# Kernel optimization log

Measured on AMD Instinct MI355X. Metric: run time of the kernel, lower is better.

## Reference

```python
import jax, jax.numpy as jnp
import numpy as np

USER_NUM = 100000
ITEM_NUM = 50000
E = 128   # embedding_size
A = 64    # attention_size
M = 8     # memory_size
B = 4096  # batch
NF = 50   # friends per user


def _l2norm(x, axis):
    # torch F.normalize(p=2): x / max(||x||, eps)
    n = jnp.sqrt(jnp.sum(x * x, axis=axis, keepdims=True))
    return x / jnp.maximum(n, 1e-12)


def setup_inputs() -> dict:
    key = jax.random.key(0)
    ks = jax.random.split(key, 9)
    u = lambda k, shape: jax.random.uniform(k, shape, jnp.float32, -0.1, 0.1)
    return {
        "input_u": jax.random.randint(ks[0], (B,), 0, USER_NUM),
        "input_i": jax.random.randint(ks[1], (B,), 0, ITEM_NUM),
        "input_uf": jax.random.randint(ks[2], (B, NF), 0, USER_NUM + 1),
        "uidW": u(ks[3], (USER_NUM + 1, E)),
        "iidW": u(ks[4], (ITEM_NUM, E)),
        "i_bias": jnp.zeros((ITEM_NUM,), jnp.float32),
        "Key": u(ks[5], (E, M)),
        "Mem": jnp.ones((M, E), jnp.float32),
        "WA": u(ks[6], (E, A)),
        "BA": jnp.zeros((A,), jnp.float32),
        "U_omega": u(ks[7], (A, 1)),
    }


def reference(input_u, input_i, input_uf, uidW, iidW, i_bias, Key, Mem, WA, BA, U_omega):
    user_num = uidW.shape[0] - 1  # padding id
    uid = uidW[input_u]                      # [B, E]
    iid = iidW[input_i]                      # [B, E]
    i_b = i_bias[input_i]                    # [B]
    fe = uidW[input_uf]                      # [B, F, E] friend embeddings
    fn = (input_uf != user_num).astype(uid.dtype)  # [B, F] valid-friend mask

    fe = fn[:, :, None] * fe
    uid_n = _l2norm(uid, axis=1)
    fe_n = _l2norm(fe, axis=2)
    cross = uid_n[:, None, :] * fe_n                     # [B, F, E]
    att_key = jnp.einsum('bfe,em->bfm', cross, Key)      # [B, F, M]
    att_mem = jax.nn.softmax(att_key, axis=0)            # softmax over batch (faithful to dim=0)
    att_mem = fn[:, :, None] * att_mem
    f1 = jnp.einsum('bfm,me->bfe', att_mem, Mem)         # [B, F, E]
    f2 = f1 * fe
    h = jax.nn.relu(jnp.einsum('bfe,ea->bfa', f2, WA) + BA)
    j = jnp.exp(jnp.einsum('bfa,ao->bfo', h, U_omega))   # [B, F, 1]
    j = fn[:, :, None] * j
    w = j / (jnp.sum(j, axis=1, keepdims=True) + 1e-8)
    friend = jnp.sum(w * f2, axis=1)                     # [B, E] (dropout p=0 -> identity)
    user = uid + friend
    score = jnp.sum(user * iid, axis=1) + i_b            # [B]
    return score
```

## Files before the change

### kernel.cpp

```cpp
#include <hip/hip_runtime.h>

#define EDIM 128
#define MDIM 8
#define ADIM 64
#define NFR  50
#define NCOL (NFR * MDIM)
#define NPART 64

typedef __attribute__((ext_vector_type(8))) short short8;
typedef __attribute__((ext_vector_type(4))) float f32x4;

__device__ __forceinline__ float waveReduceSum(float v) {
    #pragma unroll
    for (int s = 32; s >= 1; s >>= 1) v += __shfl_xor(v, s, 64);
    return v;
}
__device__ __forceinline__ short f2bf(float x) {
    unsigned u = __float_as_uint(x);
    u += 0x7FFFu + ((u >> 16) & 1u);
    return (short)(u >> 16);
}
__device__ __forceinline__ float bf2f(short s) {
    return __uint_as_float(((unsigned)(unsigned short)s) << 16);
}

__global__ __launch_bounds__(256)
void k0_prep(const float* __restrict__ WA, const float* __restrict__ Mem,
             const float* __restrict__ Key,
             short* __restrict__ WATf, short* __restrict__ MemTf,
             short* __restrict__ KeyTf, float* __restrict__ S)
{
    int t = blockIdx.x * 256 + threadIdx.x;
    int lane = t & 63, c = lane & 15, g = (lane >> 4) & 3;
    short8 v = {0, 0, 0, 0, 0, 0, 0, 0};
    if (t < 1024) {
        int frag = t >> 6, Ma = frag >> 2, Kt = frag & 3;
        int a = Ma * 16 + c;
        #pragma unroll
        for (int j = 0; j < 8; ++j) {
            int e = Kt * 32 + g * 8 + j;
            v[j] = f2bf(WA[(size_t)e * ADIM + a]);
        }
        *(short8*)(WATf + (size_t)t * 8) = v;
    } else if (t < 1536) {
        int i = t - 1024, Mt = i >> 6;
        int e = Mt * 16 + c;
        #pragma unroll
        for (int j = 0; j < 8; ++j) {
            int k = g * 8 + j;
            v[j] = (k < MDIM) ? f2bf(Mem[(size_t)k * EDIM + e]) : (short)0;
        }
        *(short8*)(MemTf + (size_t)i * 8) = v;
    } else if (t < 1792) {
        int i = t - 1536, Kt = i >> 6;
        #pragma unroll
        for (int j = 0; j < 8; ++j) {
            int e = Kt * 32 + g * 8 + j;
            v[j] = (c < MDIM) ? f2bf(Key[(size_t)e * MDIM + c]) : (short)0;
        }
        *(short8*)(KeyTf + (size_t)i * 8) = v;
    } else if (t < 1792 + NCOL) {
        S[t - 1792] = 0.f;
    }
}

__global__ __launch_bounds__(256, 6)
void k1_attkey(const int* __restrict__ input_u, const int* __restrict__ input_uf,
               const float* __restrict__ uidW, const short* __restrict__ KeyTf,
               float* __restrict__ eatt, short* __restrict__ feB, int user_num)
{
    const int b = blockIdx.x, t = threadIdx.x, w = t >> 6, l = t & 63;
    const int c = l & 15, g = l >> 4;
    __shared__ float uidn[EDIM];
    __shared__ float redW[4];
    __shared__ int ufL[64];

    if (t < 64) ufL[t] = (t < NFR) ? input_uf[(size_t)b * NFR + t] : user_num;
    const int u = input_u[b];
    float x = (t < EDIM) ? uidW[(size_t)u * EDIM + t] : 0.f;
    float ss = waveReduceSum(x * x);
    if (l == 0) redW[w] = ss;
    __syncthreads();
    float uinv = 1.0f / fmaxf(sqrtf(redW[0] + redW[1] + redW[2] + redW[3]), 1e-12f);
    if (t < EDIM) uidn[t] = x * uinv;
    __syncthreads();

    const int f = w * 16 + c;
    const int fid = ufL[f];
    const float fn = (f < NFR && fid != user_num) ? 1.0f : 0.0f;
    const float* fp = uidW + (size_t)fid * EDIM;

    float4 fe[4][2];
    #pragma unroll
    for (int Kt = 0; Kt < 4; ++Kt) {
        fe[Kt][0] = *(const float4*)(fp + Kt * 32 + g * 8);
        fe[Kt][1] = *(const float4*)(fp + Kt * 32 + g * 8 + 4);
    }
    float fss = 0.f;
    #pragma unroll
    for (int Kt = 0; Kt < 4; ++Kt)
        #pragma unroll
        for (int h = 0; h < 2; ++h) {
            float4 q = fe[Kt][h];
            fss += q.x * q.x + q.y * q.y + q.z * q.z + q.w * q.w;
        }
    fss += __shfl_xor(fss, 16, 64);
    fss += __shfl_xor(fss, 32, 64);
    const float inv2 = fn / fmaxf(sqrtf(fss), 1e-12f);

    short* fbb = feB + (size_t)b * 8192;
    f32x4 acc = {0.f, 0.f, 0.f, 0.f};
    #pragma unroll
    for (int Kt = 0; Kt < 4; ++Kt) {
        short8 fo;
        fo[0] = f2bf(fe[Kt][0].x * fn); fo[1] = f2bf(fe[Kt][0].y * fn);
        fo[2] = f2bf(fe[Kt][0].z * fn); fo[3] = f2bf(fe[Kt][0].w * fn);
        fo[4] = f2bf(fe[Kt][1].x * fn); fo[5] = f2bf(fe[Kt][1].y * fn);
        fo[6] = f2bf(fe[Kt][1].z * fn); fo[7] = f2bf(fe[Kt][1].w * fn);
        *(short8*)(fbb + f * 128 + Kt * 32 + g * 8) = fo;

        float4 un0 = *(const float4*)&uidn[Kt * 32 + g * 8];
        float4 un1 = *(const float4*)&uidn[Kt * 32 + g * 8 + 4];
        short8 bf;
        bf[0] = f2bf(un0.x * fe[Kt][0].x * inv2);
        bf[1] = f2bf(un0.y * fe[Kt][0].y * inv2);
        bf[2] = f2bf(un0.z * fe[Kt][0].z * inv2);
        bf[3] = f2bf(un0.w * fe[Kt][0].w * inv2);
        bf[4] = f2bf(un1.x * fe[Kt][1].x * inv2);
        bf[5] = f2bf(un1.y * fe[Kt][1].y * inv2);
        bf[6] = f2bf(un1.z * fe[Kt][1].z * inv2);
        bf[7] = f2bf(un1.w * fe[Kt][1].w * inv2);
        short8 af = *(const short8*)(KeyTf + (size_t)(Kt * 64 + l) * 8);
        acc = __builtin_amdgcn_mfma_f32_16x16x32_bf16(af, bf, acc, 0, 0, 0);
    }
    if (f < NFR && g < 2) {
        float4 st = {__expf(acc[0]), __expf(acc[1]), __expf(acc[2]), __expf(acc[3])};
        *(float4*)&eatt[(size_t)b * NCOL + f * MDIM + g * 4] = st;
    }
}

__global__ __launch_bounds__(256)
void k2a_sum(const float* __restrict__ eatt, float* __restrict__ S, int B)
{
    const int blk = blockIdx.x, t = threadIdx.x, w = t >> 6, l = t & 63;
    __shared__ float colS[4][NCOL];
    const int rowsPerBlk = B / NPART;
    const int rowsPerWave = rowsPerBlk >> 2;
    const int r0 = blk * rowsPerBlk + w * rowsPerWave;

    float4 a1 = {0.f, 0.f, 0.f, 0.f}, a2 = {0.f, 0.f, 0.f, 0.f};
    for (int it = 0; it < rowsPerWave; ++it) {
        const float* row = eatt + (size_t)(r0 + it) * NCOL;
        float4 v1 = *(const float4*)(row + 4 * l);
        a1.x += v1.x; a1.y += v1.y; a1.z += v1.z; a1.w += v1.w;
        if (l < 36) {
            float4 v2 = *(const float4*)(row + 256 + 4 * l);
            a2.x += v2.x; a2.y += v2.y; a2.z += v2.z; a2.w += v2.w;
        }
    }
    *(float4*)&colS[w][4 * l] = a1;
    if (l < 36) *(float4*)&colS[w][256 + 4 * l] = a2;
    __syncthreads();
    for (int i = t; i < NCOL; i += 256)
        atomicAdd(&S[i], colS[0][i] + colS[1][i] + colS[2][i] + colS[3][i]);
}

__global__ __launch_bounds__(256, 6)
void k3_final(const int* __restrict__ input_u, const int* __restrict__ input_i,
              const int* __restrict__ input_uf, const float* __restrict__ uidW,
              const float* __restrict__ iidW, const float* __restrict__ i_bias,
              const short* __restrict__ WATf, const short* __restrict__ MemTf,
              const float* __restrict__ BA, const float* __restrict__ U_omega,
              const float* __restrict__ eatt, const float* __restrict__ S,
              const short* __restrict__ feB, float* __restrict__ out,
              int user_num)
{
    const int b = blockIdx.x, t = threadIdx.x, w = t >> 6, l = t & 63;
    const int c = l & 15, g = l >> 4;
    __shared__ short f2s[4][4 * 64 * 8];
    __shared__ float uidL[EDIM], iidL[EDIM];
    __shared__ float baL[ADIM], uoL[ADIM];
    __shared__ int ufL[64];
    __shared__ float sjW[4], syW[4];

    if (t < 64) ufL[t] = (t < NFR) ? input_uf[(size_t)b * NFR + t] : user_num;
    const int u = input_u[b];
    const int ii = input_i[b];
    if (t < EDIM) {
        uidL[t] = uidW[(size_t)u * EDIM + t];
        iidL[t] = iidW[(size_t)ii * EDIM + t];
    }
    if (t < ADIM) { baL[t] = BA[t]; uoL[t] = U_omega[t]; }
    __syncthreads();

    const int f = w * 16 + c;
    const float fn = (f < NFR && ufL[f] != user_num) ? 1.0f : 0.0f;
    const short* fbb = feB + (size_t)b * 8192;

    short8 amf = {0, 0, 0, 0, 0, 0, 0, 0};
    if (g == 0 && fn > 0.f) {
        const float* ea = eatt + (size_t)b * NCOL + f * 8;
        float4 e0 = *(const float4*)ea;
        float4 e1 = *(const float4*)(ea + 4);
        float4 s0 = *(const float4*)&S[f * 8];
        float4 s1 = *(const float4*)&S[f * 8 + 4];
        amf[0] = f2bf(e0.x * __builtin_amdgcn_rcpf(s0.x));
        amf[1] = f2bf(e0.y * __builtin_amdgcn_rcpf(s0.y));
        amf[2] = f2bf(e0.z * __builtin_amdgcn_rcpf(s0.z));
        amf[3] = f2bf(e0.w * __builtin_amdgcn_rcpf(s0.w));
        amf[4] = f2bf(e1.x * __builtin_amdgcn_rcpf(s1.x));
        amf[5] = f2bf(e1.y * __builtin_amdgcn_rcpf(s1.y));
        amf[6] = f2bf(e1.z * __builtin_amdgcn_rcpf(s1.z));
        amf[7] = f2bf(e1.w * __builtin_amdgcn_rcpf(s1.w));
    }

    f32x4 C1[8];
    #pragma unroll
    for (int Mt = 0; Mt < 8; ++Mt) {
        short8 af = *(const short8*)(MemTf + (size_t)(Mt * 64 + l) * 8);
        f32x4 z = {0.f, 0.f, 0.f, 0.f};
        C1[Mt] = __builtin_amdgcn_mfma_f32_16x16x32_bf16(af, amf, z, 0, 0, 0);
    }

    #pragma unroll
    for (int Mt = 0; Mt < 8; ++Mt) {
        uint2 fv = *(const uint2*)(fbb + f * 128 + Mt * 16 + g * 4);
        float q0 = C1[Mt][0] * bf2f((short)(fv.x & 0xFFFF));
        float q1 = C1[Mt][1] * bf2f((short)(fv.x >> 16));
        float q2 = C1[Mt][2] * bf2f((short)(fv.y & 0xFFFF));
        float q3 = C1[Mt][3] * bf2f((short)(fv.y >> 16));
        unsigned d0 = ((unsigned)(unsigned short)f2bf(q0)) |
                      (((unsigned)(unsigned short)f2bf(q1)) << 16);
        unsigned d1 = ((unsigned)(unsigned short)f2bf(q2)) |
                      (((unsigned)(unsigned short)f2bf(q3)) << 16);
        int lane2 = ((Mt & 1) * 2 + (g >> 1)) * 16 + c;
        int off = ((Mt >> 1) * 64 + lane2) * 8 + (g & 1) * 4;
        uint2 dd = {d0, d1};
        *(uint2*)&f2s[w][off] = dd;
    }

    f32x4 C2[4], C3 = {0.f, 0.f, 0.f, 0.f};
    #pragma unroll
    for (int Ma = 0; Ma < 4; ++Ma) C2[Ma] = (f32x4){0.f, 0.f, 0.f, 0.f};
    #pragma unroll
    for (int Kt = 0; Kt < 4; ++Kt) {
        short8 bf = *(const short8*)&f2s[w][(Kt * 64 + l) * 8];
        #pragma unroll
        for (int Ma = 0; Ma < 4; ++Ma) {
            short8 af = *(const short8*)(WATf + (size_t)((Ma * 4 + Kt) * 64 + l) * 8);
            C2[Ma] = __builtin_amdgcn_mfma_f32_16x16x32_bf16(af, bf, C2[Ma], 0, 0, 0);
        }
        short8 itf = {0, 0, 0, 0, 0, 0, 0, 0};
        if (c == 0) {
            float4 i0 = *(const float4*)&iidL[Kt * 32 + g * 8];
            float4 i1 = *(const float4*)&iidL[Kt * 32 + g * 8 + 4];
            itf[0] = f2bf(i0.x); itf[1] = f2bf(i0.y);
            itf[2] = f2bf(i0.z); itf[3] = f2bf(i0.w);
            itf[4] = f2bf(i1.x); itf[5] = f2bf(i1.y);
            itf[6] = f2bf(i1.z); itf[7] = f2bf(i1.w);
        }
        C3 = __builtin_amdgcn_mfma_f32_16x16x32_bf16(itf, bf, C3, 0, 0, 0);
    }

    float psum = 0.f;
    #pragma unroll
    for (int Ma = 0; Ma < 4; ++Ma) {
        float4 ba4 = *(const float4*)&baL[Ma * 16 + g * 4];
        float4 uo4 = *(const float4*)&uoL[Ma * 16 + g * 4];
        psum += fmaxf(C2[Ma][0] + ba4.x, 0.f) * uo4.x;
        psum += fmaxf(C2[Ma][1] + ba4.y, 0.f) * uo4.y;
        psum += fmaxf(C2[Ma][2] + ba4.z, 0.f) * uo4.z;
        psum += fmaxf(C2[Ma][3] + ba4.w, 0.f) * uo4.w;
    }
    psum += __shfl_xor(psum, 16, 64);
    psum += __shfl_xor(psum, 32, 64);
    const float jv = (fn > 0.f) ? __expf(psum) : 0.f;
    const float jy = jv * C3[0];
    float sj = waveReduceSum((g == 0) ? jv : 0.f);
    float sy = waveReduceSum(jy);
    if (l == 0) { sjW[w] = sj; syW[w] = sy; }
    __syncthreads();

    if (w == 0) {
        float s = uidL[l] * iidL[l] + uidL[l + 64] * iidL[l + 64];
        s = waveReduceSum(s);
        if (l == 0) {
            float Sj = sjW[0] + sjW[1] + sjW[2] + sjW[3] + 1e-8f;
            float Sy = syW[0] + syW[1] + syW[2] + syW[3];
            out[b] = s + Sy / Sj + i_bias[ii];
        }
    }
}

extern "C" void kernel_launch(void* const* d_in, const int* in_sizes, int n_in,
                              void* d_out, int out_size, void* d_ws, size_t ws_size,
                              hipStream_t stream)
{
    const int*   input_u  = (const int*)d_in[0];
    const int*   input_i  = (const int*)d_in[1];
    const int*   input_uf = (const int*)d_in[2];
    const float* uidW     = (const float*)d_in[3];
    const float* iidW     = (const float*)d_in[4];
    const float* i_bias   = (const float*)d_in[5];
    const float* Key      = (const float*)d_in[6];
    const float* Mem      = (const float*)d_in[7];
    const float* WA       = (const float*)d_in[8];
    const float* BA       = (const float*)d_in[9];
    const float* U_om     = (const float*)d_in[10];

    const int B = in_sizes[0];
    const int user_num = in_sizes[3] / EDIM - 1;

    float* eatt = (float*)d_ws;
    float* S    = eatt + (size_t)B * NCOL;
    short* WATf  = (short*)(S + NCOL);
    short* MemTf = WATf + 16 * 64 * 8;
    short* KeyTf = MemTf + 8 * 64 * 8;
    short* feB   = KeyTf + 4 * 64 * 8;

    k0_prep<<<9, 256, 0, stream>>>(WA, Mem, Key, WATf, MemTf, KeyTf, S);
    k1_attkey<<<B, 256, 0, stream>>>(input_u, input_uf, uidW, KeyTf, eatt, feB, user_num);
    k2a_sum<<<NPART, 256, 0, stream>>>(eatt, S, B);
    k3_final<<<B, 256, 0, stream>>>(input_u, input_i, input_uf, uidW, iidW, i_bias,
                                    WATf, MemTf, BA, U_om, eatt, S, feB,
                                    (float*)d_out, user_num);
}
```

Before: 187.9 us.

## Pre-convert user embedding table to bf16 and gather from it instead of staging feB

A new prep stage converts the whole user embedding table to bf16 on every call. Both the attention-key kernel and the final kernel then gather friend embeddings directly from that bf16 table. This removes the large per-batch feB buffer that one kernel wrote and the other read back, and it halves the bytes of every gather. In exchange, each call streams the full table once for conversion, and the user's own embedding is now read in bf16, which slightly lowers precision. The occupancy hint for k1 also goes from 6 to 8.

```diff
diff --git a/kernel.cpp b/kernel.cpp
--- a/kernel.cpp
+++ b/kernel.cpp
@@ -25,12 +25,26 @@
 }
 
 __global__ __launch_bounds__(256)
-void k0_prep(const float* __restrict__ WA, const float* __restrict__ Mem,
-             const float* __restrict__ Key,
-             short* __restrict__ WATf, short* __restrict__ MemTf,
-             short* __restrict__ KeyTf, float* __restrict__ S)
-{
-    int t = blockIdx.x * 256 + threadIdx.x;
+void k0_all(const float* __restrict__ uidW, const float* __restrict__ WA,
+            const float* __restrict__ Mem, const float* __restrict__ Key,
+            short* __restrict__ ubW, short* __restrict__ WATf,
+            short* __restrict__ MemTf, short* __restrict__ KeyTf,
+            float* __restrict__ S, int nU, int cvtBlocks)
+{
+    int blk = blockIdx.x;
+    if (blk < cvtBlocks) {
+        int idx = (blk * 256 + threadIdx.x) * 8;
+        if (idx < nU) {
+            float4 a = *(const float4*)(uidW + idx);
+            float4 b = *(const float4*)(uidW + idx + 4);
+            short8 v;
+            v[0] = f2bf(a.x); v[1] = f2bf(a.y); v[2] = f2bf(a.z); v[3] = f2bf(a.w);
+            v[4] = f2bf(b.x); v[5] = f2bf(b.y); v[6] = f2bf(b.z); v[7] = f2bf(b.w);
+            *(short8*)(ubW + idx) = v;
+        }
+        return;
+    }
+    int t = (blk - cvtBlocks) * 256 + threadIdx.x;
     int lane = t & 63, c = lane & 15, g = (lane >> 4) & 3;
     short8 v = {0, 0, 0, 0, 0, 0, 0, 0};
     if (t < 1024) {
@@ -64,10 +78,10 @@
     }
 }
 
-__global__ __launch_bounds__(256, 6)
+__global__ __launch_bounds__(256, 8)
 void k1_attkey(const int* __restrict__ input_u, const int* __restrict__ input_uf,
-               const float* __restrict__ uidW, const short* __restrict__ KeyTf,
-               float* __restrict__ eatt, short* __restrict__ feB, int user_num)
+               const short* __restrict__ ubW, const short* __restrict__ KeyTf,
+               float* __restrict__ eatt, int user_num)
 {
     const int b = blockIdx.x, t = threadIdx.x, w = t >> 6, l = t & 63;
     const int c = l & 15, g = l >> 4;
@@ -77,7 +91,7 @@
 
     if (t < 64) ufL[t] = (t < NFR) ? input_uf[(size_t)b * NFR + t] : user_num;
     const int u = input_u[b];
-    float x = (t < EDIM) ? uidW[(size_t)u * EDIM + t] : 0.f;
+    float x = (t < EDIM) ? bf2f(ubW[(size_t)u * EDIM + t]) : 0.f;
     float ss = waveReduceSum(x * x);
     if (l == 0) redW[w] = ss;
     __syncthreads();
@@ -88,48 +102,35 @@
     const int f = w * 16 + c;
     const int fid = ufL[f];
     const float fn = (f < NFR && fid != user_num) ? 1.0f : 0.0f;
-    const float* fp = uidW + (size_t)fid * EDIM;
-
-    float4 fe[4][2];
-    #pragma unroll
-    for (int Kt = 0; Kt < 4; ++Kt) {
-        fe[Kt][0] = *(const float4*)(fp + Kt * 32 + g * 8);
-        fe[Kt][1] = *(const float4*)(fp + Kt * 32 + g * 8 + 4);
-    }
+    const short* fp = ubW + (size_t)fid * EDIM;
+
+    short8 feb[4];
+    #pragma unroll
+    for (int Kt = 0; Kt < 4; ++Kt)
+        feb[Kt] = *(const short8*)(fp + Kt * 32 + g * 8);
+
+    float fef[4][8];
     float fss = 0.f;
     #pragma unroll
     for (int Kt = 0; Kt < 4; ++Kt)
         #pragma unroll
-        for (int h = 0; h < 2; ++h) {
-            float4 q = fe[Kt][h];
-            fss += q.x * q.x + q.y * q.y + q.z * q.z + q.w * q.w;
+        for (int j = 0; j < 8; ++j) {
+            float q = bf2f(feb[Kt][j]);
+            fef[Kt][j] = q;
+            fss += q * q;
         }
     fss += __shfl_xor(fss, 16, 64);
     fss += __shfl_xor(fss, 32, 64);
     const float inv2 = fn / fmaxf(sqrtf(fss), 1e-12f);
 
-    short* fbb = feB + (size_t)b * 8192;
     f32x4 acc = {0.f, 0.f, 0.f, 0.f};
     #pragma unroll
     for (int Kt = 0; Kt < 4; ++Kt) {
-        short8 fo;
-        fo[0] = f2bf(fe[Kt][0].x * fn); fo[1] = f2bf(fe[Kt][0].y * fn);
-        fo[2] = f2bf(fe[Kt][0].z * fn); fo[3] = f2bf(fe[Kt][0].w * fn);
-        fo[4] = f2bf(fe[Kt][1].x * fn); fo[5] = f2bf(fe[Kt][1].y * fn);
-        fo[6] = f2bf(fe[Kt][1].z * fn); fo[7] = f2bf(fe[Kt][1].w * fn);
-        *(short8*)(fbb + f * 128 + Kt * 32 + g * 8) = fo;
-
-        float4 un0 = *(const float4*)&uidn[Kt * 32 + g * 8];
-        float4 un1 = *(const float4*)&uidn[Kt * 32 + g * 8 + 4];
+        const float* un = &uidn[Kt * 32 + g * 8];
         short8 bf;
-        bf[0] = f2bf(un0.x * fe[Kt][0].x * inv2);
-        bf[1] = f2bf(un0.y * fe[Kt][0].y * inv2);
-        bf[2] = f2bf(un0.z * fe[Kt][0].z * inv2);
-        bf[3] = f2bf(un0.w * fe[Kt][0].w * inv2);
-        bf[4] = f2bf(un1.x * fe[Kt][1].x * inv2);
-        bf[5] = f2bf(un1.y * fe[Kt][1].y * inv2);
-        bf[6] = f2bf(un1.z * fe[Kt][1].z * inv2);
-        bf[7] = f2bf(un1.w * fe[Kt][1].w * inv2);
+        #pragma unroll
+        for (int j = 0; j < 8; ++j)
+            bf[j] = f2bf(un[j] * fef[Kt][j] * inv2);
         short8 af = *(const short8*)(KeyTf + (size_t)(Kt * 64 + l) * 8);
         acc = __builtin_amdgcn_mfma_f32_16x16x32_bf16(af, bf, acc, 0, 0, 0);
     }
@@ -172,7 +173,7 @@
               const short* __restrict__ WATf, const short* __restrict__ MemTf,
               const float* __restrict__ BA, const float* __restrict__ U_omega,
               const float* __restrict__ eatt, const float* __restrict__ S,
-              const short* __restrict__ feB, float* __restrict__ out,
+              const short* __restrict__ ubW, float* __restrict__ out,
               int user_num)
 {
     const int b = blockIdx.x, t = threadIdx.x, w = t >> 6, l = t & 63;
@@ -194,8 +195,9 @@
     __syncthreads();
 
     const int f = w * 16 + c;
-    const float fn = (f < NFR && ufL[f] != user_num) ? 1.0f : 0.0f;
-    const short* fbb = feB + (size_t)b * 8192;
+    const int fid = ufL[f];
+    const float fn = (f < NFR && fid != user_num) ? 1.0f : 0.0f;
+    const short* fp3 = ubW + (size_t)fid * EDIM;
 
     short8 amf = {0, 0, 0, 0, 0, 0, 0, 0};
     if (g == 0 && fn > 0.f) {
@@ -224,7 +226,7 @@
 
     #pragma unroll
     for (int Mt = 0; Mt < 8; ++Mt) {
-        uint2 fv = *(const uint2*)(fbb + f * 128 + Mt * 16 + g * 4);
+        uint2 fv = *(const uint2*)(fp3 + Mt * 16 + g * 4);
         float q0 = C1[Mt][0] * bf2f((short)(fv.x & 0xFFFF));
         float q1 = C1[Mt][1] * bf2f((short)(fv.x >> 16));
         float q2 = C1[Mt][2] * bf2f((short)(fv.y & 0xFFFF));
@@ -309,19 +311,23 @@
     const float* U_om     = (const float*)d_in[10];
 
     const int B = in_sizes[0];
-    const int user_num = in_sizes[3] / EDIM - 1;
+    const int nU = in_sizes[3];
+    const int user_num = nU / EDIM - 1;
 
     float* eatt = (float*)d_ws;
     float* S    = eatt + (size_t)B * NCOL;
     short* WATf  = (short*)(S + NCOL);
     short* MemTf = WATf + 16 * 64 * 8;
     short* KeyTf = MemTf + 8 * 64 * 8;
-    short* feB   = KeyTf + 4 * 64 * 8;
-
-    k0_prep<<<9, 256, 0, stream>>>(WA, Mem, Key, WATf, MemTf, KeyTf, S);
-    k1_attkey<<<B, 256, 0, stream>>>(input_u, input_uf, uidW, KeyTf, eatt, feB, user_num);
+    short* ubW   = KeyTf + 4 * 64 * 8;
+
+    const int cvtBlocks = (nU / 8 + 255) / 256;
+    k0_all<<<cvtBlocks + 9, 256, 0, stream>>>(uidW, WA, Mem, Key,
+                                              ubW, WATf, MemTf, KeyTf, S,
+                                              nU, cvtBlocks);
+    k1_attkey<<<B, 256, 0, stream>>>(input_u, input_uf, ubW, KeyTf, eatt, user_num);
     k2a_sum<<<NPART, 256, 0, stream>>>(eatt, S, B);
     k3_final<<<B, 256, 0, stream>>>(input_u, input_i, input_uf, uidW, iidW, i_bias,
-                                    WATf, MemTf, BA, U_om, eatt, S, feB,
+                                    WATf, MemTf, BA, U_om, eatt, S, ubW,
                                     (float*)d_out, user_num);
 }
```

New measurement: 173.8 us. 7.6% less time.
